# Kernel optimization log

Hardware: AMD Instinct MI355X
Metric: run time of the kernel (lower is better)

The kernel has to match this reference:

```python
import jax, jax.numpy as jnp
import numpy as np

C = 768        # n_embd
HSZ = 64       # HEAD_SIZE (module-level global in source)
H = C // HSZ   # n_head = 12
G = 2          # conv groups
DL = HSZ       # D_MIX_LORA = HEAD_SIZE
DD = 64        # TIME_DECAY_DIM
DG = C // 4    # D_GATE_LORA
B, T = 2, 2048

PNAMES = ['time_maa_x','time_maa_r','time_maa_w','time_maa_k','time_maa_v','time_maa_a','time_maa_g',
          'time_decay','time_faaaa','time_aaaaa','maa_w1','maa_w2','decay_w1','decay_w2','aaa_w1','aaa_w2',
          'kkk_w1','kkk_w2','gate_w1','gate_w2','w_key','w_value','w_receptance','w_output','ln_x_weight']

def setup_inputs() -> dict:
    key = jax.random.key(0)
    ks = jax.random.split(key, 32)
    f = lambda i, shape, s=1.0: jax.random.normal(ks[i], shape, jnp.float32) * s
    u = lambda i, shape: jax.random.uniform(ks[i], shape, dtype=jnp.float32)
    cs = float(C // G) ** -0.5
    return dict(
        x=f(0, (B, C, T)),
        time_maa_x=u(1, (1, C, 1)), time_maa_r=u(2, (1, C, 1)), time_maa_w=u(3, (1, C, 1)),
        time_maa_k=u(4, (1, C, 1)), time_maa_v=u(5, (1, C, 1)), time_maa_a=u(6, (1, C, 1)),
        time_maa_g=u(7, (1, C, 1)),
        time_decay=f(8, (1, C, 1), 0.5), time_faaaa=f(9, (H, HSZ), 0.1), time_aaaaa=f(10, (1, C, 1), 0.1),
        maa_w1=f(11, (6 * DL, C), 0.02), maa_w2=f(12, (6, DL, C), 0.02),
        decay_w1=f(13, (DD, C), 0.02), decay_w2=f(14, (C, DD), 0.02),
        aaa_w1=f(15, (DD, C), 0.02), aaa_w2=f(16, (C, DD), 0.02),
        kkk_w1=f(17, (DD, C), 0.02), kkk_w2=f(18, (C, DD), 0.02),
        gate_w1=f(19, (DG, C), 0.02), gate_w2=f(20, (C, DG), 0.02),
        w_key=f(21, (G, C // G, C // G), cs), w_value=f(22, (G, C // G, C // G), cs),
        w_receptance=f(23, (G, C // G, C // G), cs), w_output=f(24, (G, C // G, C // G), cs),
        ln_x_weight=jnp.ones((C,), jnp.float32),
    )

def _gconv(x, w):
    # grouped 1x1 Conv1d: x (B,C,T), w (G, C/G out, C/G in) -> (B,C,T)
    b, c, t = x.shape
    xg = x.reshape(b, G, c // G, t)
    return jnp.einsum('goc,bgct->bgot', w, xg).reshape(b, c, t)

def _lora(w1, w2, z):
    # w2 @ tanh(w1 @ z), channels-first z (B,C,T)
    return jnp.einsum('cd,bdt->bct', w2, jnp.tanh(jnp.einsum('dc,bct->bdt', w1, z)))

def _wkv7(r, w, k, v, a, bb):
    # RWKV-7 generalized delta-rule recurrence. All inputs (B,T,C), w in log-decay space.
    b, t, c = r.shape
    rs = lambda x: jnp.moveaxis(x.reshape(b, t, H, HSZ), 1, 0)  # (T,B,H,N)
    r4, k4, v4, a4, b4 = map(rs, (r, k, v, a, bb))
    wdec = rs(jnp.exp(-jnp.exp(w)))
    def step(S, inp):
        rr, ww, kk, vv, aa, b2 = inp  # each (B,H,N)
        sab = jnp.einsum('bhij,bhj,bhk->bhik', S, aa, b2)
        S = S * ww[:, :, None, :] + sab + vv[..., None] * kk[:, :, None, :]
        y = jnp.einsum('bhij,bhj->bhi', S, rr)
        return S, y
    S0 = jnp.zeros((b, H, HSZ, HSZ), r.dtype)
    _, ys = jax.lax.scan(step, S0, (r4, wdec, k4, v4, a4, b4))
    return jnp.moveaxis(ys, 0, 1).reshape(b, t, c)

def _forward(x, time_maa_x, time_maa_r, time_maa_w, time_maa_k, time_maa_v, time_maa_a, time_maa_g,
             time_decay, time_faaaa, time_aaaaa, maa_w1, maa_w2, decay_w1, decay_w2, aaa_w1, aaa_w2,
             kkk_w1, kkk_w2, gate_w1, gate_w2, w_key, w_value, w_receptance, w_output, ln_x_weight):
    b, c, t = x.shape
    xx = x  # shift_mode == 'none'
    xm = x * time_maa_x + xx * (1.0 - time_maa_x)
    tm = jnp.tanh(jnp.einsum('dc,bct->bdt', maa_w1, xm)).reshape(b, 6, DL, t)
    mix = jnp.einsum('bndt,ndc->nbct', tm, maa_w2)  # (6,B,C,T)
    mr, mw, mk, mv, ma, mg = mix
    xr = x + xx * (time_maa_r + mr)
    xw = x + xx * (time_maa_w + mw)
    xk = x + xx * (time_maa_k + mk)
    xv = x + xx * (time_maa_v + mv)
    xa = x + xx * (time_maa_a + ma)
    xg = x + xx * (time_maa_g + mg)
    tr = lambda z: z.transpose(0, 2, 1)  # (B,C,T) -> (B,T,C)
    r = tr(_gconv(xr, w_receptance))
    wlog = tr(-jax.nn.softplus(-(time_decay + _lora(decay_w1, decay_w2, xw))) - 0.5)
    k = tr(_gconv(xk, w_key))
    v = tr(_gconv(xv, w_value))
    g = tr(_lora(gate_w1, gate_w2, xg))
    kk = k + tr(_lora(kkk_w1, kkk_w2, xk))
    kk4 = kk.reshape(b, t, H, HSZ)
    kk = (kk4 / jnp.maximum(jnp.linalg.norm(kk4, axis=-1, keepdims=True), 1e-12)).reshape(b, t, c)
    a = jax.nn.sigmoid(tr(time_aaaaa + _lora(aaa_w1, aaa_w2, xa)))
    y = _wkv7(r, wlog, k, v, -kk, kk * a)
    # ln_x: RMSNorm over channel dim
    y = y * jax.lax.rsqrt(jnp.mean(y * y, axis=-1, keepdims=True) + 1e-5) * ln_x_weight
    rk = (r.reshape(b, t, H, HSZ) * k.reshape(b, t, H, HSZ) * time_faaaa).sum(-1, keepdims=True)
    y = y + (rk * v.reshape(b, t, H, HSZ)).reshape(b, t, c)
    return _gconv(tr(y * g), w_output)  # (B,C,T)

def reference(x, time_maa_x, time_maa_r, time_maa_w, time_maa_k, time_maa_v, time_maa_a, time_maa_g,
              time_decay, time_faaaa, time_aaaaa, maa_w1, maa_w2, decay_w1, decay_w2, aaa_w1, aaa_w2,
              kkk_w1, kkk_w2, gate_w1, gate_w2, w_key, w_value, w_receptance, w_output, ln_x_weight):
    return _forward(x, time_maa_x, time_maa_r, time_maa_w, time_maa_k, time_maa_v, time_maa_a, time_maa_g,
                    time_decay, time_faaaa, time_aaaaa, maa_w1, maa_w2, decay_w1, decay_w2, aaa_w1, aaa_w2,
                    kkk_w1, kkk_w2, gate_w1, gate_w2, w_key, w_value, w_receptance, w_output, ln_x_weight)
```

## Files before the change

kernel.cpp:

```cpp
#include <hip/hip_runtime.h>
#include <math.h>

#define BB 2
#define TT 2048
#define CC 768
#define HH 12
#define NN 64
#define GG 2
#define CG 384
#define FF 3145728L
#define S1 1572864L

typedef __attribute__((ext_vector_type(8))) short bf8frag;
typedef __attribute__((ext_vector_type(4))) float f4acc;

__device__ inline unsigned short f2bf(float x) {
    union { float f; unsigned u; } v; v.f = x;
    unsigned r = v.u + 0x7FFFu + ((v.u >> 16) & 1u);
    return (unsigned short)(r >> 16);
}
__device__ inline float bf2f(unsigned short u) {
    union { unsigned u; float f; } v; v.u = ((unsigned)u) << 16;
    return v.f;
}

template<int ATRANS, int BTRANS, int TOUT, int MODE>
__global__ __launch_bounds__(256) void gemm_kernel(
    const float* __restrict__ A, const float* __restrict__ Bm, float* __restrict__ Cm,
    const float* __restrict__ aux, const float* __restrict__ aux2,
    int K, int ldA, int ldB, int ldC, int zInner,
    long sA_o, long sA_i, long sB_o, long sB_i, long sC_o, long sC_i,
    long sAux_i, long sAux2_o, unsigned short* bfout)
{
    const int zo = blockIdx.z / zInner;
    const int zi = blockIdx.z % zInner;
    A  += (size_t)zo * sA_o + (size_t)zi * sA_i;
    Bm += (size_t)zo * sB_o + (size_t)zi * sB_i;
    Cm += (size_t)zo * sC_o + (size_t)zi * sC_i;
    if (MODE == 2) { aux += (size_t)zi * sAux_i; aux2 += (size_t)zo * sAux2_o; }

    const int m0t = blockIdx.y * 64;
    const int n0t = blockIdx.x * 64;
    const int tid = threadIdx.x;

    __shared__ float As[16][64];
    __shared__ float Bs[16][64];

    int mi, ni;
    if (TOUT) { mi = (tid & 15) * 4; ni = (tid >> 4) * 4; }
    else      { ni = (tid & 15) * 4; mi = (tid >> 4) * 4; }

    float acc[4][4];
#pragma unroll
    for (int i = 0; i < 4; ++i)
#pragma unroll
        for (int j = 0; j < 4; ++j) acc[i][j] = 0.f;

    for (int k0 = 0; k0 < K; k0 += 16) {
        if (!ATRANS) {
            const int row = tid >> 2;
            const int kc  = (tid & 3) * 4;
            float4 av = *(const float4*)&A[(size_t)(m0t + row) * ldA + k0 + kc];
            As[kc + 0][row] = av.x; As[kc + 1][row] = av.y;
            As[kc + 2][row] = av.z; As[kc + 3][row] = av.w;
        } else {
            const int krow = tid >> 4;
            const int mc   = (tid & 15) * 4;
            *(float4*)&As[krow][mc] = *(const float4*)&A[(size_t)(k0 + krow) * ldA + m0t + mc];
        }
        if (!BTRANS) {
            const int krow = tid >> 4;
            const int tc   = (tid & 15) * 4;
            *(float4*)&Bs[krow][tc] = *(const float4*)&Bm[(size_t)(k0 + krow) * ldB + n0t + tc];
        } else {
            const int trow = tid >> 2;
            const int kc   = (tid & 3) * 4;
            float4 bv = *(const float4*)&Bm[(size_t)(n0t + trow) * ldB + k0 + kc];
            Bs[kc + 0][trow] = bv.x; Bs[kc + 1][trow] = bv.y;
            Bs[kc + 2][trow] = bv.z; Bs[kc + 3][trow] = bv.w;
        }
        __syncthreads();
#pragma unroll
        for (int kk = 0; kk < 16; ++kk) {
            float4 a4 = *(const float4*)&As[kk][mi];
            float4 b4 = *(const float4*)&Bs[kk][ni];
            float am[4] = {a4.x, a4.y, a4.z, a4.w};
            float bn[4] = {b4.x, b4.y, b4.z, b4.w};
#pragma unroll
            for (int i = 0; i < 4; ++i)
#pragma unroll
                for (int j = 0; j < 4; ++j) acc[i][j] = fmaf(am[i], bn[j], acc[i][j]);
        }
        __syncthreads();
    }

    const int mbase = m0t + mi, nbase = n0t + ni;
#pragma unroll
    for (int i = 0; i < 4; ++i) {
        float4 xv;
        if (MODE == 2) xv = *(const float4*)&aux2[(size_t)(mbase + i) * ldC + nbase];
        float xa[4] = {0.f, 0.f, 0.f, 0.f};
        if (MODE == 2) { xa[0] = xv.x; xa[1] = xv.y; xa[2] = xv.z; xa[3] = xv.w; }
#pragma unroll
        for (int j = 0; j < 4; ++j) {
            float v = acc[i][j];
            if (MODE == 1) v = tanhf(v);
            else if (MODE == 2) v = xa[j] * (aux[mbase + i] + v);
            else if (MODE == 3) {
                float u  = aux[mbase + i] + v;
                float sp = fmaxf(-u, 0.f) + log1pf(expf(-fabsf(u)));
                float wl = -sp - 0.5f;
                v = expf(-expf(wl));
            } else if (MODE == 4) {
                float u = aux[mbase + i] + v;
                v = 1.f / (1.f + expf(-u));
            }
            acc[i][j] = v;
        }
    }
    if (!TOUT) {
        const bool skipf = (MODE == 2) && (bfout != nullptr) && (zi == 0 || zi == 3);
        if (!skipf) {
#pragma unroll
            for (int i = 0; i < 4; ++i) {
                float4 o = {acc[i][0], acc[i][1], acc[i][2], acc[i][3]};
                *(float4*)&Cm[(size_t)(mbase + i) * ldC + nbase] = o;
            }
        }
        if (MODE == 2 && bfout != nullptr) {
            int sidx = (zi == 0) ? 0 : (zi == 2) ? 1 : (zi == 3) ? 2 : -1;
            if (sidx >= 0) {
                unsigned short* bp = bfout + (size_t)sidx * FF + (size_t)zo * ((long)CC * TT);
#pragma unroll
                for (int i = 0; i < 4; ++i) {
                    ushort4 o = {f2bf(acc[i][0]), f2bf(acc[i][1]), f2bf(acc[i][2]), f2bf(acc[i][3])};
                    *(ushort4*)&bp[(size_t)(mbase + i) * ldC + nbase] = o;
                }
            }
        }
    } else {
#pragma unroll
        for (int j = 0; j < 4; ++j) {
            float4 o = {acc[0][j], acc[1][j], acc[2][j], acc[3][j]};
            *(float4*)&Cm[(size_t)(nbase + j) * ldC + mbase] = o;
        }
    }
}

__global__ __launch_bounds__(256) void lorah_kernel(
    const float* __restrict__ w0, const float* __restrict__ w1,
    const float* __restrict__ w2, const float* __restrict__ w3,
    const float* __restrict__ x0, const float* __restrict__ x1,
    const float* __restrict__ x2, const float* __restrict__ x3,
    float* __restrict__ o0, float* __restrict__ o1,
    float* __restrict__ o2, float* __restrict__ o3)
{
    const int z = blockIdx.z;
    const int which = z >> 1, bz = z & 1;
    if (which < 3 && blockIdx.y > 0) return;
    const float* A; const float* Bm; float* Cm; int M;
    if (which == 0)      { A = w0; Bm = x0; Cm = o0; M = 64; }
    else if (which == 1) { A = w1; Bm = x1; Cm = o1; M = 64; }
    else if (which == 2) { A = w2; Bm = x2; Cm = o2; M = 64; }
    else                 { A = w3; Bm = x3; Cm = o3; M = 192; }
    Bm += (size_t)bz * ((long)CC * TT);
    Cm += (size_t)bz * ((long)M * TT);

    const int m0t = blockIdx.y * 64;
    const int n0t = blockIdx.x * 64;
    const int tid = threadIdx.x;

    __shared__ float As[16][64];
    __shared__ float Bs[16][64];

    const int ni = (tid & 15) * 4, mi = (tid >> 4) * 4;
    float acc[4][4];
#pragma unroll
    for (int i = 0; i < 4; ++i)
#pragma unroll
        for (int j = 0; j < 4; ++j) acc[i][j] = 0.f;

    for (int k0 = 0; k0 < CC; k0 += 16) {
        {
            const int row = tid >> 2, kc = (tid & 3) * 4;
            float4 av = *(const float4*)&A[(size_t)(m0t + row) * CC + k0 + kc];
            As[kc + 0][row] = av.x; As[kc + 1][row] = av.y;
            As[kc + 2][row] = av.z; As[kc + 3][row] = av.w;
        }
        {
            const int krow = tid >> 4, tc = (tid & 15) * 4;
            *(float4*)&Bs[krow][tc] = *(const float4*)&Bm[(size_t)(k0 + krow) * TT + n0t + tc];
        }
        __syncthreads();
#pragma unroll
        for (int kk = 0; kk < 16; ++kk) {
            float4 a4 = *(const float4*)&As[kk][mi];
            float4 b4 = *(const float4*)&Bs[kk][ni];
            float am[4] = {a4.x, a4.y, a4.z, a4.w};
            float bn[4] = {b4.x, b4.y, b4.z, b4.w};
#pragma unroll
            for (int i = 0; i < 4; ++i)
#pragma unroll
                for (int j = 0; j < 4; ++j) acc[i][j] = fmaf(am[i], bn[j], acc[i][j]);
        }
        __syncthreads();
    }
    const int mbase = m0t + mi, nbase = n0t + ni;
#pragma unroll
    for (int i = 0; i < 4; ++i) {
        float4 o = {tanhf(acc[i][0]), tanhf(acc[i][1]), tanhf(acc[i][2]), tanhf(acc[i][3])};
        *(float4*)&Cm[(size_t)(mbase + i) * TT + nbase] = o;
    }
}

__global__ __launch_bounds__(256) void convs3_mfma_kernel(
    const unsigned short* __restrict__ wball, const unsigned short* __restrict__ X6t,
    float* __restrict__ X6)
{
    const int z = blockIdx.z;
    const int conv = z >> 2, bg = z & 3, b = bg >> 1, g = bg & 1;
    const unsigned short* Wb = wball + (size_t)conv * 294912;
    const unsigned short* Xb = X6t + (size_t)conv * FF;
    const int oslot = (conv == 0) ? 1 : (conv == 1) ? 4 : 5;
    float* Cout = X6 + (size_t)oslot * FF;

    const int t0 = blockIdx.x * 128;
    const int m0 = blockIdx.y * 128;
    const int tid = threadIdx.x;
    const int wave = tid >> 6, lane = tid & 63;
    const int lq = lane >> 4, lr = lane & 15;

    __shared__ unsigned short Ws[128 * 40];
    __shared__ unsigned short Xs[128 * 40];

    const unsigned short* Wg = Wb + (size_t)g * (CG * CG);
    const long xbase = (long)b * (long)TT * CC;

    f4acc acc0[8], acc1[8];
#pragma unroll
    for (int j = 0; j < 8; ++j) { acc0[j] = (f4acc)0.f; acc1[j] = (f4acc)0.f; }

    for (int k0 = 0; k0 < CG; k0 += 32) {
        {
            const int m = tid >> 1, kc = (tid & 1) * 16;
            const unsigned short* src = Wg + (size_t)(m0 + m) * CG + k0 + kc;
            *(bf8frag*)&Ws[m * 40 + kc]     = *(const bf8frag*)src;
            *(bf8frag*)&Ws[m * 40 + kc + 8] = *(const bf8frag*)(src + 8);
        }
        {
            const int t = tid >> 1, kc = (tid & 1) * 16;
            const unsigned short* src = Xb + xbase + (long)(t0 + t) * CC + g * CG + k0 + kc;
            *(bf8frag*)&Xs[t * 40 + kc]     = *(const bf8frag*)src;
            *(bf8frag*)&Xs[t * 40 + kc + 8] = *(const bf8frag*)(src + 8);
        }
        __syncthreads();

        bf8frag a0 = *(const bf8frag*)&Ws[(32 * wave + lr) * 40 + lq * 8];
        bf8frag a1 = *(const bf8frag*)&Ws[(32 * wave + 16 + lr) * 40 + lq * 8];
#pragma unroll
        for (int nj = 0; nj < 8; ++nj) {
            bf8frag bb = *(const bf8frag*)&Xs[(16 * nj + lr) * 40 + lq * 8];
            acc0[nj] = __builtin_amdgcn_mfma_f32_16x16x32_bf16(a0, bb, acc0[nj], 0, 0, 0);
            acc1[nj] = __builtin_amdgcn_mfma_f32_16x16x32_bf16(a1, bb, acc1[nj], 0, 0, 0);
        }
        __syncthreads();
    }

#pragma unroll
    for (int fi = 0; fi < 2; ++fi) {
        const int cbase = m0 + 32 * wave + 16 * fi + lq * 4;
#pragma unroll
        for (int nj = 0; nj < 8; ++nj) {
            const f4acc av = fi ? acc1[nj] : acc0[nj];
            const int t = t0 + 16 * nj + lr;
            float4 o = {av[0], av[1], av[2], av[3]};
            *(float4*)&Cout[(long)b * (long)TT * CC + (long)t * CC + g * CG + cbase] = o;
        }
    }
}

__global__ __launch_bounds__(256) void convout_mfma_kernel(
    const unsigned short* __restrict__ Wb, const unsigned short* __restrict__ Xb,
    float* __restrict__ Cout)
{
    const int bz = blockIdx.z; const int b = bz >> 1, g = bz & 1;
    const int t0 = blockIdx.x * 128;
    const int m0 = blockIdx.y * 128;
    const int tid = threadIdx.x;
    const int wave = tid >> 6, lane = tid & 63;
    const int lq = lane >> 4, lr = lane & 15;

    __shared__ unsigned short Ws[128 * 40];
    __shared__ unsigned short Xs[128 * 40];

    const unsigned short* Wg = Wb + (size_t)g * (CG * CG);
    const long xbase = (long)b * (long)TT * CC;

    f4acc acc0[8], acc1[8];
#pragma unroll
    for (int j = 0; j < 8; ++j) { acc0[j] = (f4acc)0.f; acc1[j] = (f4acc)0.f; }

    for (int k0 = 0; k0 < CG; k0 += 32) {
        {
            const int m = tid >> 1, kc = (tid & 1) * 16;
            const unsigned short* src = Wg + (size_t)(m0 + m) * CG + k0 + kc;
            *(bf8frag*)&Ws[m * 40 + kc]     = *(const bf8frag*)src;
            *(bf8frag*)&Ws[m * 40 + kc + 8] = *(const bf8frag*)(src + 8);
        }
        {
            const int t = tid >> 1, kc = (tid & 1) * 16;
            const unsigned short* src = Xb + xbase + (long)(t0 + t) * CC + g * CG + k0 + kc;
            *(bf8frag*)&Xs[t * 40 + kc]     = *(const bf8frag*)src;
            *(bf8frag*)&Xs[t * 40 + kc + 8] = *(const bf8frag*)(src + 8);
        }
        __syncthreads();

        bf8frag a0 = *(const bf8frag*)&Ws[(32 * wave + lr) * 40 + lq * 8];
        bf8frag a1 = *(const bf8frag*)&Ws[(32 * wave + 16 + lr) * 40 + lq * 8];
#pragma unroll
        for (int nj = 0; nj < 8; ++nj) {
            bf8frag bb = *(const bf8frag*)&Xs[(16 * nj + lr) * 40 + lq * 8];
            acc0[nj] = __builtin_amdgcn_mfma_f32_16x16x32_bf16(a0, bb, acc0[nj], 0, 0, 0);
            acc1[nj] = __builtin_amdgcn_mfma_f32_16x16x32_bf16(a1, bb, acc1[nj], 0, 0, 0);
        }
        __syncthreads();
    }

#pragma unroll
    for (int fi = 0; fi < 2; ++fi) {
        const int cbase = m0 + 32 * wave + 16 * fi + lq * 4;
#pragma unroll
        for (int nj = 0; nj < 8; ++nj) {
            const f4acc av = fi ? acc1[nj] : acc0[nj];
            const int t = t0 + 16 * nj + lr;
#pragma unroll
            for (int i = 0; i < 4; ++i)
                Cout[(long)b * (long)CC * TT + (long)(g * CG + cbase + i) * TT + t] = av[i];
        }
    }
}

__global__ __launch_bounds__(256) void maaw1_mfma_kernel(
    const unsigned short* __restrict__ Wb, const unsigned short* __restrict__ Xb,
    float* __restrict__ Cout)
{
    const int b = blockIdx.z;
    const int t0 = blockIdx.x * 128;
    const int m0 = blockIdx.y * 128;
    const int tid = threadIdx.x;
    const int wave = tid >> 6, lane = tid & 63;
    const int lq = lane >> 4, lr = lane & 15;

    __shared__ unsigned short Ws[128 * 40];
    __shared__ unsigned short Xs[128 * 40];

    const long xbase = (long)b * (long)TT * CC;

    f4acc acc0[8], acc1[8];
#pragma unroll
    for (int j = 0; j < 8; ++j) { acc0[j] = (f4acc)0.f; acc1[j] = (f4acc)0.f; }

    for (int k0 = 0; k0 < CC; k0 += 32) {
        {
            const int m = tid >> 1, kc = (tid & 1) * 16;
            const unsigned short* src = Wb + (size_t)(m0 + m) * CC + k0 + kc;
            *(bf8frag*)&Ws[m * 40 + kc]     = *(const bf8frag*)src;
            *(bf8frag*)&Ws[m * 40 + kc + 8] = *(const bf8frag*)(src + 8);
        }
        {
            const int t = tid >> 1, kc = (tid & 1) * 16;
            const unsigned short* src = Xb + xbase + (long)(t0 + t) * CC + k0 + kc;
            *(bf8frag*)&Xs[t * 40 + kc]     = *(const bf8frag*)src;
            *(bf8frag*)&Xs[t * 40 + kc + 8] = *(const bf8frag*)(src + 8);
        }
        __syncthreads();

        bf8frag a0 = *(const bf8frag*)&Ws[(32 * wave + lr) * 40 + lq * 8];
        bf8frag a1 = *(const bf8frag*)&Ws[(32 * wave + 16 + lr) * 40 + lq * 8];
#pragma unroll
        for (int nj = 0; nj < 8; ++nj) {
            bf8frag bb = *(const bf8frag*)&Xs[(16 * nj + lr) * 40 + lq * 8];
            acc0[nj] = __builtin_amdgcn_mfma_f32_16x16x32_bf16(a0, bb, acc0[nj], 0, 0, 0);
            acc1[nj] = __builtin_amdgcn_mfma_f32_16x16x32_bf16(a1, bb, acc1[nj], 0, 0, 0);
        }
        __syncthreads();
    }

#pragma unroll
    for (int fi = 0; fi < 2; ++fi) {
        const int m = m0 + 32 * wave + 16 * fi + lq * 4;
#pragma unroll
        for (int nj = 0; nj < 8; ++nj) {
            const f4acc av = fi ? acc1[nj] : acc0[nj];
            const int t = t0 + 16 * nj + lr;
#pragma unroll
            for (int i = 0; i < 4; ++i)
                Cout[(long)b * 384 * TT + (long)(m + i) * TT + t] = tanhf(av[i]);
        }
    }
}

__global__ __launch_bounds__(256) void xtr_kernel(const float* __restrict__ xin,
                                                  unsigned short* __restrict__ xout)
{
    __shared__ unsigned short L[64][68];
    const int t0 = blockIdx.x * 64, c0 = blockIdx.y * 64, b = blockIdx.z;
    const int tid = threadIdx.x;
    const int lr = tid >> 4, lc = (tid & 15) * 4;
#pragma unroll
    for (int i = 0; i < 4; ++i) {
        int c = lr + i * 16;
        float4 v = *(const float4*)&xin[(size_t)b * CC * TT + (size_t)(c0 + c) * TT + t0 + lc];
        L[c][lc + 0] = f2bf(v.x); L[c][lc + 1] = f2bf(v.y);
        L[c][lc + 2] = f2bf(v.z); L[c][lc + 3] = f2bf(v.w);
    }
    __syncthreads();
#pragma unroll
    for (int i = 0; i < 4; ++i) {
        int t = lr + i * 16;
        ushort4 o = {L[lc + 0][t], L[lc + 1][t], L[lc + 2][t], L[lc + 3][t]};
        *(ushort4*)&xout[(size_t)b * TT * CC + (size_t)(t0 + t) * CC + c0 + lc] = o;
    }
}

__global__ __launch_bounds__(256) void btr_kernel(const unsigned short* __restrict__ xin,
                                                  unsigned short* __restrict__ xout)
{
    __shared__ unsigned short L[64][68];
    const int t0 = blockIdx.x * 64, c0 = blockIdx.y * 64;
    const int s = blockIdx.z >> 1, b = blockIdx.z & 1;
    const int tid = threadIdx.x;
    const int lr = tid >> 4, lc = (tid & 15) * 4;
    const size_t ibase = (size_t)s * FF + (size_t)b * CC * TT;
    const size_t obase = (size_t)s * FF + (size_t)b * TT * CC;
#pragma unroll
    for (int i = 0; i < 4; ++i) {
        int c = lr + i * 16;
        ushort4 v = *(const ushort4*)&xin[ibase + (size_t)(c0 + c) * TT + t0 + lc];
        L[c][lc + 0] = v.x; L[c][lc + 1] = v.y; L[c][lc + 2] = v.z; L[c][lc + 3] = v.w;
    }
    __syncthreads();
#pragma unroll
    for (int i = 0; i < 4; ++i) {
        int t = lr + i * 16;
        ushort4 o = {L[lc + 0][t], L[lc + 1][t], L[lc + 2][t], L[lc + 3][t]};
        *(ushort4*)&xout[obase + (size_t)(t0 + t) * CC + c0 + lc] = o;
    }
}

__global__ void wcvt_kernel(const float* __restrict__ w0, const float* __restrict__ w1,
                            const float* __restrict__ w2, const float* __restrict__ w3,
                            const float* __restrict__ w4, unsigned short* __restrict__ wb)
{
    const int i = blockIdx.x * 256 + threadIdx.x;
    const int which = i / 294912, r = i - which * 294912;
    const float* s = (which == 0) ? w0 : (which == 1) ? w1 : (which == 2) ? w2
                   : (which == 3) ? w3 : w4;
    wb[i] = f2bf(s[r]);
}

__global__ void pack_aux_kernel(const float* __restrict__ r, const float* __restrict__ w,
                                const float* __restrict__ k, const float* __restrict__ v,
                                const float* __restrict__ a, const float* __restrict__ g,
                                float* __restrict__ paux)
{
    int c = blockIdx.x * blockDim.x + threadIdx.x;
    if (c < CC) {
        paux[0 * CC + c] = 1.f + r[c];
        paux[1 * CC + c] = 1.f + w[c];
        paux[2 * CC + c] = 1.f + k[c];
        paux[3 * CC + c] = 1.f + v[c];
        paux[4 * CC + c] = 1.f + a[c];
        paux[5 * CC + c] = 1.f + g[c];
    }
}

__global__ __launch_bounds__(256) void e1_kernel(const float* __restrict__ kA,
                                                 float* __restrict__ kvecA,
                                                 float* __restrict__ aA)
{
    const size_t base = (size_t)blockIdx.x * CC;
    const int tid = threadIdx.x;
#pragma unroll
    for (int ch = 0; ch < 3; ++ch) {
        int c = ch * 256 + tid;
        float kk = kA[base + c] + kvecA[base + c];
        float ss = kk * kk;
#pragma unroll
        for (int off = 32; off; off >>= 1) ss += __shfl_xor(ss, off, 64);
        float denom = fmaxf(sqrtf(ss), 1e-12f);
        float kkn = kk / denom;
        float av = aA[base + c];
        kvecA[base + c] = -kkn;
        aA[base + c]    = kkn * av;
    }
}

struct WFrag {
    float4 w[2], a[2], b[2], k[2], r[2];
    float vv;
};

__global__ __launch_bounds__(64) void wkv_kernel(
    const float* __restrict__ rA, const float* __restrict__ wA,
    const float* __restrict__ kA, const float* __restrict__ vA,
    const float* __restrict__ aaA, const float* __restrict__ b2A,
    unsigned short* __restrict__ yp8)
{
    const int blk = blockIdx.x;
    const int bh = blk % 24, rg = blk / 24;
    const int b = bh / HH, h = bh - b * HH;
    const int lane = threadIdx.x;
    const int jg = lane >> 3, p = lane & 7;
    const int row = rg * 8 + p;
    const int base = b * TT * CC + h * NN;
    const int fo = jg * 8;
    const int ybase = (jg * BB + b) * (TT * CC) + h * NN + row;

    float S[8];
#pragma unroll
    for (int i = 0; i < 8; ++i) S[i] = 0.f;

    WFrag f0, f1, f2;

    auto loadfrag = [&](WFrag& f, int t) {
        const int o = base + t * CC + fo;
#pragma unroll
        for (int q = 0; q < 2; ++q) {
            f.w[q] = *(const float4*)&wA[o + 4 * q];
            f.a[q] = *(const float4*)&aaA[o + 4 * q];
            f.b[q] = *(const float4*)&b2A[o + 4 * q];
            f.k[q] = *(const float4*)&kA[o + 4 * q];
            f.r[q] = *(const float4*)&rA[o + 4 * q];
        }
        f.vv = vA[base + t * CC + row];
    };

    auto stepf = [&](const WFrag& f, int t) {
        const float vv = f.vv;
        float vk[8];
#pragma unroll
        for (int q = 0; q < 2; ++q) {
            vk[4*q+0] = vv * f.k[q].x;
            vk[4*q+1] = vv * f.k[q].y;
            vk[4*q+2] = vv * f.k[q].z;
            vk[4*q+3] = vv * f.k[q].w;
        }

        float t0 = 0.f, t1 = 0.f, t2 = 0.f, t3 = 0.f;
#pragma unroll
        for (int q = 0; q < 2; ++q) {
            float4 a4 = f.a[q];
            t0 = fmaf(S[4*q+0], a4.x, t0);
            t1 = fmaf(S[4*q+1], a4.y, t1);
            t2 = fmaf(S[4*q+2], a4.z, t2);
            t3 = fmaf(S[4*q+3], a4.w, t3);
        }
        float part = (t0 + t1) + (t2 + t3);
        float s08 = __shfl_xor(part,  8, 64);
        float s16 = __shfl_xor(part, 16, 64);
        float s24 = __shfl_xor(part, 24, 64);
        float s32 = __shfl_xor(part, 32, 64);
        float s40 = __shfl_xor(part, 40, 64);
        float s48 = __shfl_xor(part, 48, 64);
        float s56 = __shfl_xor(part, 56, 64);
        float tmp = ((part + s08) + (s16 + s24)) + ((s32 + s40) + (s48 + s56));

        float y0 = 0.f, y1 = 0.f, y2 = 0.f, y3 = 0.f;
#pragma unroll
        for (int q = 0; q < 2; ++q) {
            float4 w4 = f.w[q], b4 = f.b[q], r4 = f.r[q];
            S[4*q+0] = fmaf(S[4*q+0], w4.x, fmaf(tmp, b4.x, vk[4*q+0]));
            y0 = fmaf(S[4*q+0], r4.x, y0);
            S[4*q+1] = fmaf(S[4*q+1], w4.y, fmaf(tmp, b4.y, vk[4*q+1]));
            y1 = fmaf(S[4*q+1], r4.y, y1);
            S[4*q+2] = fmaf(S[4*q+2], w4.z, fmaf(tmp, b4.z, vk[4*q+2]));
            y2 = fmaf(S[4*q+2], r4.z, y2);
            S[4*q+3] = fmaf(S[4*q+3], w4.w, fmaf(tmp, b4.w, vk[4*q+3]));
            y3 = fmaf(S[4*q+3], r4.w, y3);
        }
        yp8[ybase + t * CC] = f2bf((y0 + y1) + (y2 + y3));
    };

    loadfrag(f0, 0);
    loadfrag(f1, 1);
    loadfrag(f2, 2);

    int t = 0;
    for (; t + 2 < TT; t += 3) {
        stepf(f0, t);
        if (t + 3 < TT) loadfrag(f0, t + 3);
        stepf(f1, t + 1);
        if (t + 4 < TT) loadfrag(f1, t + 4);
        stepf(f2, t + 2);
        if (t + 5 < TT) loadfrag(f2, t + 5);
    }
    if (t < TT) stepf(f0, t);
    if (t + 1 < TT) stepf(f1, t + 1);
}

__global__ __launch_bounds__(256) void e2_kernel(
    const unsigned short* __restrict__ yp8, const float* __restrict__ rA,
    const float* __restrict__ kA, const float* __restrict__ vA,
    const float* __restrict__ gA, const float* __restrict__ faaaa,
    const float* __restrict__ lnw, unsigned short* __restrict__ zB)
{
    const int bt = blockIdx.x;
    const int b = bt / TT, t = bt - b * TT;
    const size_t base = (size_t)bt * CC;
    const int tid = threadIdx.x;
    const int wave = tid >> 6;
    __shared__ float red[4];
    __shared__ float rk[12];

    float yv[3];
    float ss = 0.f;
#pragma unroll
    for (int ch = 0; ch < 3; ++ch) {
        int c = ch * 256 + tid;
        float y = 0.f;
#pragma unroll
        for (int jg = 0; jg < 8; ++jg)
            y += bf2f(yp8[((size_t)(jg * BB + b) * TT + t) * CC + c]);
        yv[ch] = y;
        ss = fmaf(y, y, ss);
        float p = rA[base + c] * kA[base + c] * faaaa[c];
#pragma unroll
        for (int off = 32; off; off >>= 1) p += __shfl_xor(p, off, 64);
        if ((tid & 63) == 0) rk[ch * 4 + wave] = p;
    }
#pragma unroll
    for (int off = 32; off; off >>= 1) ss += __shfl_xor(ss, off, 64);
    if ((tid & 63) == 0) red[wave] = ss;
    __syncthreads();
    const float total = red[0] + red[1] + red[2] + red[3];
    const float scale = rsqrtf(total / (float)CC + 1e-5f);
#pragma unroll
    for (int ch = 0; ch < 3; ++ch) {
        int c = ch * 256 + tid;
        float out = yv[ch] * scale * lnw[c] + rk[c >> 6] * vA[base + c];
        zB[base + c] = f2bf(out * gA[base + c]);
    }
}

extern "C" void kernel_launch(void* const* d_in, const int* in_sizes, int n_in,
                              void* d_out, int out_size, void* d_ws, size_t ws_size,
                              hipStream_t stream)
{
    (void)in_sizes; (void)n_in; (void)out_size; (void)ws_size;
    const float* x        = (const float*)d_in[0];
    const float* tmaa_r   = (const float*)d_in[2];
    const float* tmaa_w   = (const float*)d_in[3];
    const float* tmaa_k   = (const float*)d_in[4];
    const float* tmaa_v   = (const float*)d_in[5];
    const float* tmaa_a   = (const float*)d_in[6];
    const float* tmaa_g   = (const float*)d_in[7];
    const float* tdecay   = (const float*)d_in[8];
    const float* tfaaaa   = (const float*)d_in[9];
    const float* taaaaa   = (const float*)d_in[10];
    const float* maa_w1   = (const float*)d_in[11];
    const float* maa_w2   = (const float*)d_in[12];
    const float* decay_w1 = (const float*)d_in[13];
    const float* decay_w2 = (const float*)d_in[14];
    const float* aaa_w1   = (const float*)d_in[15];
    const float* aaa_w2   = (const float*)d_in[16];
    const float* kkk_w1   = (const float*)d_in[17];
    const float* kkk_w2   = (const float*)d_in[18];
    const float* gate_w1  = (const float*)d_in[19];
    const float* gate_w2  = (const float*)d_in[20];
    const float* w_key    = (const float*)d_in[21];
    const float* w_value  = (const float*)d_in[22];
    const float* w_recept = (const float*)d_in[23];
    const float* w_output = (const float*)d_in[24];
    const float* lnw      = (const float*)d_in[25];
    float* out = (float*)d_out;

    float* ws   = (float*)d_ws;
    float* paux = ws;
    float* tm   = ws + 8192;
    float* X6   = tm + S1;
    float* dh   = X6 + 6 * FF;
    float* ah   = dh + 262144;
    float* kh   = ah + 262144;
    float* gh   = kh + 262144;
    float* gbuf = gh + 786432;
    unsigned short* yp8 = (unsigned short*)(gbuf + FF);
    unsigned short* X6b = yp8 + 8 * FF;
    unsigned short* zb  = X6b + 3 * FF;
    unsigned short* wb  = zb + FF;
    unsigned short* xtb = wb + 5L * 294912;
    unsigned short* X6t = xtb + FF;

    float* xw = X6 + 1 * FF; float* xk = X6 + 2 * FF;
    float* xa = X6 + 4 * FF; float* xg = X6 + 5 * FF;
    float* wwB = X6 + 0 * FF; float* rB  = X6 + 1 * FF; float* aaB = X6 + 2 * FF;
    float* b2B = X6 + 3 * FF; float* kB  = X6 + 4 * FF; float* vB  = X6 + 5 * FF;

    const long CT = (long)CC * TT;
    const long TC = (long)TT * CC;

    pack_aux_kernel<<<dim3(3), 256, 0, stream>>>(tmaa_r, tmaa_w, tmaa_k, tmaa_v, tmaa_a, tmaa_g, paux);
    wcvt_kernel<<<dim3(5760), 256, 0, stream>>>(w_recept, w_key, w_value, w_output, maa_w1, wb);
    xtr_kernel<<<dim3(32, 12, 2), 256, 0, stream>>>(x, xtb);

    maaw1_mfma_kernel<<<dim3(16, 3, 2), 256, 0, stream>>>(wb + 4L * 294912, xtb, tm);

    gemm_kernel<1,0,0,2><<<dim3(32, 12, 12), 256, 0, stream>>>(
        maa_w2, tm, X6, paux, x,
        64, 768, TT, TT, 6,
        0, 64L * 768, 384L * TT, 64L * TT, CT, FF, 768, CT, X6b);

    btr_kernel<<<dim3(32, 12, 6), 256, 0, stream>>>(X6b, X6t);

    lorah_kernel<<<dim3(32, 3, 8), 256, 0, stream>>>(
        decay_w1, aaa_w1, kkk_w1, gate_w1, xw, xa, xk, xg, dh, ah, kh, gh);

    convs3_mfma_kernel<<<dim3(16, 3, 12), 256, 0, stream>>>(wb, X6t, X6);

    gemm_kernel<0,0,1,3><<<dim3(32, 12, 2), 256, 0, stream>>>(
        decay_w2, dh, wwB, tdecay, nullptr, 64, 64, TT, CC, 1,
        0, 0, 64L * TT, 0, TC, 0, 0, 0, nullptr);
    gemm_kernel<0,0,1,4><<<dim3(32, 12, 2), 256, 0, stream>>>(
        aaa_w2, ah, b2B , taaaaa, nullptr, 64, 64, TT, CC, 1,
        0, 0, 64L * TT, 0, TC, 0, 0, 0, nullptr);
    gemm_kernel<0,0,1,0><<<dim3(32, 12, 2), 256, 0, stream>>>(
        kkk_w2, kh, aaB , nullptr, nullptr, 64, 64, TT, CC, 1,
        0, 0, 64L * TT, 0, TC, 0, 0, 0, nullptr);
    gemm_kernel<0,0,1,0><<<dim3(32, 12, 2), 256, 0, stream>>>(
        gate_w2, gh, gbuf, nullptr, nullptr, 192, 192, TT, CC, 1,
        0, 0, 192L * TT, 0, TC, 0, 0, 0, nullptr);

    e1_kernel<<<dim3(BB * TT), 256, 0, stream>>>(kB, aaB, b2B);

    wkv_kernel<<<dim3(BB * HH * 8), 64, 0, stream>>>(rB, wwB, kB, vB, aaB, b2B, yp8);

    e2_kernel<<<dim3(BB * TT), 256, 0, stream>>>(yp8, rB, kB, vB, gbuf, tfaaaa, lnw, zb);

    convout_mfma_kernel<<<dim3(16, 3, 4), 256, 0, stream>>>(wb + 3L * 294912, zb, out);
}
```

Measured before the change: 866.7 us.

## Move WKV state-dot reduction off the serial critical path via precomputed scalars

Rewrites the WKV recurrence so the cross-lane reduction S·a for the next step is computed from the pre-update state (with w and the next step's a folded in). The current step's tmp is then rebuilt from precomputed per-head scalars beta=b_{t-1}·a_t and gamma=k_{t-1}·a_t, which a new bg_kernel produces. This removes the shuffle reduction latency from the dependency chain between consecutive timesteps, so it can overlap with the state update. In exchange it adds an extra kernel launch and an extra pass over b, a and k, and reassociates floating-point sums.

```diff
diff --git a/kernel.cpp b/kernel.cpp
--- a/kernel.cpp
+++ b/kernel.cpp
@@ -496,15 +496,48 @@
     }
 }
 
+__global__ __launch_bounds__(256) void bg_kernel(
+    const float* __restrict__ b2A, const float* __restrict__ aaA,
+    const float* __restrict__ kA, float2* __restrict__ bgout)
+{
+    const int bt = blockIdx.x;
+    const int b = bt / TT, t = bt - b * TT;
+    const int tid = threadIdx.x;
+    const size_t base  = (size_t)bt * CC;
+    const size_t basep = base - CC;
+#pragma unroll
+    for (int ch = 0; ch < 3; ++ch) {
+        int c = ch * 256 + tid;
+        int h = c >> 6;
+        float pb = 0.f, pk = 0.f;
+        if (t > 0) {
+            float av = aaA[base + c];
+            pb = b2A[basep + c] * av;
+            pk = kA[basep + c] * av;
+        }
+#pragma unroll
+        for (int off = 32; off; off >>= 1) {
+            pb += __shfl_xor(pb, off, 64);
+            pk += __shfl_xor(pk, off, 64);
+        }
+        if ((tid & 63) == 0) {
+            float2 o; o.x = pb; o.y = pk;
+            bgout[(size_t)(b * HH + h) * TT + t] = o;
+        }
+    }
+}
+
 struct WFrag {
-    float4 w[2], a[2], b[2], k[2], r[2];
+    float4 a[2], w[2], b[2], k[2], r[2];
     float vv;
+    float beta, gamma;
 };
 
 __global__ __launch_bounds__(64) void wkv_kernel(
     const float* __restrict__ rA, const float* __restrict__ wA,
     const float* __restrict__ kA, const float* __restrict__ vA,
     const float* __restrict__ aaA, const float* __restrict__ b2A,
+    const float2* __restrict__ bgA,
     unsigned short* __restrict__ yp8)
 {
     const int blk = blockIdx.x;
@@ -516,19 +549,24 @@
     const int base = b * TT * CC + h * NN;
     const int fo = jg * 8;
     const int ybase = (jg * BB + b) * (TT * CC) + h * NN + row;
+    const float2* bgp = bgA + (size_t)bh * TT;
 
     float S[8];
 #pragma unroll
     for (int i = 0; i < 8; ++i) S[i] = 0.f;
+
+    float tmp_prev = 0.f, v_prev = 0.f, u_cur = 0.f;
 
     WFrag f0, f1, f2;
 
     auto loadfrag = [&](WFrag& f, int t) {
         const int o = base + t * CC + fo;
+        float2 bg2 = bgp[t];
+        f.beta = bg2.x; f.gamma = bg2.y;
 #pragma unroll
         for (int q = 0; q < 2; ++q) {
+            f.a[q] = *(const float4*)&aaA[o + 4 * q];
             f.w[q] = *(const float4*)&wA[o + 4 * q];
-            f.a[q] = *(const float4*)&aaA[o + 4 * q];
             f.b[q] = *(const float4*)&b2A[o + 4 * q];
             f.k[q] = *(const float4*)&kA[o + 4 * q];
             f.r[q] = *(const float4*)&rA[o + 4 * q];
@@ -536,49 +574,45 @@
         f.vv = vA[base + t * CC + row];
     };
 
-    auto stepf = [&](const WFrag& f, int t) {
+    auto stepf = [&](const WFrag& f, const WFrag& fn, int t) {
+        const float tmp = fmaf(f.beta, tmp_prev, fmaf(f.gamma, v_prev, u_cur));
         const float vv = f.vv;
-        float vk[8];
+
+        float ua0 = 0.f, ua1 = 0.f, ua2 = 0.f, ua3 = 0.f;
 #pragma unroll
         for (int q = 0; q < 2; ++q) {
-            vk[4*q+0] = vv * f.k[q].x;
-            vk[4*q+1] = vv * f.k[q].y;
-            vk[4*q+2] = vv * f.k[q].z;
-            vk[4*q+3] = vv * f.k[q].w;
-        }
-
-        float t0 = 0.f, t1 = 0.f, t2 = 0.f, t3 = 0.f;
+            const float4 w4 = f.w[q], an4 = fn.a[q];
+            ua0 = fmaf(S[4*q+0], w4.x * an4.x, ua0);
+            ua1 = fmaf(S[4*q+1], w4.y * an4.y, ua1);
+            ua2 = fmaf(S[4*q+2], w4.z * an4.z, ua2);
+            ua3 = fmaf(S[4*q+3], w4.w * an4.w, ua3);
+        }
+        const float upart = (ua0 + ua1) + (ua2 + ua3);
+        float s08 = __shfl_xor(upart,  8, 64);
+        float s16 = __shfl_xor(upart, 16, 64);
+        float s24 = __shfl_xor(upart, 24, 64);
+        float s32 = __shfl_xor(upart, 32, 64);
+        float s40 = __shfl_xor(upart, 40, 64);
+        float s48 = __shfl_xor(upart, 48, 64);
+        float s56 = __shfl_xor(upart, 56, 64);
+
+        float y0 = 0.f, y1 = 0.f, y2 = 0.f, y3 = 0.f;
 #pragma unroll
         for (int q = 0; q < 2; ++q) {
-            float4 a4 = f.a[q];
-            t0 = fmaf(S[4*q+0], a4.x, t0);
-            t1 = fmaf(S[4*q+1], a4.y, t1);
-            t2 = fmaf(S[4*q+2], a4.z, t2);
-            t3 = fmaf(S[4*q+3], a4.w, t3);
-        }
-        float part = (t0 + t1) + (t2 + t3);
-        float s08 = __shfl_xor(part,  8, 64);
-        float s16 = __shfl_xor(part, 16, 64);
-        float s24 = __shfl_xor(part, 24, 64);
-        float s32 = __shfl_xor(part, 32, 64);
-        float s40 = __shfl_xor(part, 40, 64);
-        float s48 = __shfl_xor(part, 48, 64);
-        float s56 = __shfl_xor(part, 56, 64);
-        float tmp = ((part + s08) + (s16 + s24)) + ((s32 + s40) + (s48 + s56));
-
-        float y0 = 0.f, y1 = 0.f, y2 = 0.f, y3 = 0.f;
-#pragma unroll
-        for (int q = 0; q < 2; ++q) {
-            float4 w4 = f.w[q], b4 = f.b[q], r4 = f.r[q];
-            S[4*q+0] = fmaf(S[4*q+0], w4.x, fmaf(tmp, b4.x, vk[4*q+0]));
+            const float4 w4 = f.w[q], b4 = f.b[q], k4 = f.k[q], r4 = f.r[q];
+            S[4*q+0] = fmaf(S[4*q+0], w4.x, fmaf(tmp, b4.x, vv * k4.x));
             y0 = fmaf(S[4*q+0], r4.x, y0);
-            S[4*q+1] = fmaf(S[4*q+1], w4.y, fmaf(tmp, b4.y, vk[4*q+1]));
+            S[4*q+1] = fmaf(S[4*q+1], w4.y, fmaf(tmp, b4.y, vv * k4.y));
             y1 = fmaf(S[4*q+1], r4.y, y1);
-            S[4*q+2] = fmaf(S[4*q+2], w4.z, fmaf(tmp, b4.z, vk[4*q+2]));
+            S[4*q+2] = fmaf(S[4*q+2], w4.z, fmaf(tmp, b4.z, vv * k4.z));
             y2 = fmaf(S[4*q+2], r4.z, y2);
-            S[4*q+3] = fmaf(S[4*q+3], w4.w, fmaf(tmp, b4.w, vk[4*q+3]));
+            S[4*q+3] = fmaf(S[4*q+3], w4.w, fmaf(tmp, b4.w, vv * k4.w));
             y3 = fmaf(S[4*q+3], r4.w, y3);
         }
+
+        u_cur = ((upart + s08) + (s16 + s24)) + ((s32 + s40) + (s48 + s56));
+        tmp_prev = tmp; v_prev = vv;
+
         yp8[ybase + t * CC] = f2bf((y0 + y1) + (y2 + y3));
     };
 
@@ -588,15 +622,15 @@
 
     int t = 0;
     for (; t + 2 < TT; t += 3) {
-        stepf(f0, t);
+        stepf(f0, f1, t);
         if (t + 3 < TT) loadfrag(f0, t + 3);
-        stepf(f1, t + 1);
+        stepf(f1, f2, t + 1);
         if (t + 4 < TT) loadfrag(f1, t + 4);
-        stepf(f2, t + 2);
+        stepf(f2, f0, t + 2);
         if (t + 5 < TT) loadfrag(f2, t + 5);
     }
-    if (t < TT) stepf(f0, t);
-    if (t + 1 < TT) stepf(f1, t + 1);
+    if (t < TT) stepf(f0, f1, t);
+    if (t + 1 < TT) stepf(f1, f2, t + 1);
 }
 
 __global__ __launch_bounds__(256) void e2_kernel(
@@ -696,6 +730,8 @@
     float* wwB = X6 + 0 * FF; float* rB  = X6 + 1 * FF; float* aaB = X6 + 2 * FF;
     float* b2B = X6 + 3 * FF; float* kB  = X6 + 4 * FF; float* vB  = X6 + 5 * FF;
 
+    float2* bgbuf = (float2*)tm;
+
     const long CT = (long)CC * TT;
     const long TC = (long)TT * CC;
 
@@ -732,7 +768,9 @@
 
     e1_kernel<<<dim3(BB * TT), 256, 0, stream>>>(kB, aaB, b2B);
 
-    wkv_kernel<<<dim3(BB * HH * 8), 64, 0, stream>>>(rB, wwB, kB, vB, aaB, b2B, yp8);
+    bg_kernel<<<dim3(BB * TT), 256, 0, stream>>>(b2B, aaB, kB, bgbuf);
+
+    wkv_kernel<<<dim3(BB * HH * 8), 64, 0, stream>>>(rB, wwB, kB, vB, aaB, b2B, bgbuf, yp8);
 
     e2_kernel<<<dim3(BB * TT), 256, 0, stream>>>(yp8, rB, kB, vB, gbuf, tfaaaa, lnw, zb);
 
```

Result: slower. 962.1 us (+11.0%).

## Overlap gate LoRA second GEMM with WKV recurrence in one launch

Applied to the files above, without the earlier changes.

The gate LoRA up-projection GEMM moves into the WKV kernel as extra blocks. The first 192 blocks run the serial recurrence on one wave each, and the remaining 768 blocks compute the gate GEMM with a simple shared-memory tiled FMA loop. This lets the latency-bound recurrence, which leaves most CUs idle, run alongside the GEMM and removes one launch. In exchange the WKV blocks now launch with 256 threads but use only 64, which changes their occupancy and register budget. The GEMM also uses a hand-written path instead of the shared gemm_kernel.

```diff
diff --git a/kernel.cpp b/kernel.cpp
--- a/kernel.cpp
+++ b/kernel.cpp
@@ -501,102 +501,162 @@
     float vv;
 };
 
-__global__ __launch_bounds__(64) void wkv_kernel(
+__global__ __launch_bounds__(256) void wkv_gate_kernel(
     const float* __restrict__ rA, const float* __restrict__ wA,
     const float* __restrict__ kA, const float* __restrict__ vA,
     const float* __restrict__ aaA, const float* __restrict__ b2A,
-    unsigned short* __restrict__ yp8)
-{
-    const int blk = blockIdx.x;
-    const int bh = blk % 24, rg = blk / 24;
-    const int b = bh / HH, h = bh - b * HH;
-    const int lane = threadIdx.x;
-    const int jg = lane >> 3, p = lane & 7;
-    const int row = rg * 8 + p;
-    const int base = b * TT * CC + h * NN;
-    const int fo = jg * 8;
-    const int ybase = (jg * BB + b) * (TT * CC) + h * NN + row;
-
-    float S[8];
-#pragma unroll
-    for (int i = 0; i < 8; ++i) S[i] = 0.f;
-
-    WFrag f0, f1, f2;
-
-    auto loadfrag = [&](WFrag& f, int t) {
-        const int o = base + t * CC + fo;
-#pragma unroll
-        for (int q = 0; q < 2; ++q) {
-            f.w[q] = *(const float4*)&wA[o + 4 * q];
-            f.a[q] = *(const float4*)&aaA[o + 4 * q];
-            f.b[q] = *(const float4*)&b2A[o + 4 * q];
-            f.k[q] = *(const float4*)&kA[o + 4 * q];
-            f.r[q] = *(const float4*)&rA[o + 4 * q];
-        }
-        f.vv = vA[base + t * CC + row];
-    };
-
-    auto stepf = [&](const WFrag& f, int t) {
-        const float vv = f.vv;
-        float vk[8];
-#pragma unroll
-        for (int q = 0; q < 2; ++q) {
-            vk[4*q+0] = vv * f.k[q].x;
-            vk[4*q+1] = vv * f.k[q].y;
-            vk[4*q+2] = vv * f.k[q].z;
-            vk[4*q+3] = vv * f.k[q].w;
-        }
-
-        float t0 = 0.f, t1 = 0.f, t2 = 0.f, t3 = 0.f;
-#pragma unroll
-        for (int q = 0; q < 2; ++q) {
-            float4 a4 = f.a[q];
-            t0 = fmaf(S[4*q+0], a4.x, t0);
-            t1 = fmaf(S[4*q+1], a4.y, t1);
-            t2 = fmaf(S[4*q+2], a4.z, t2);
-            t3 = fmaf(S[4*q+3], a4.w, t3);
-        }
-        float part = (t0 + t1) + (t2 + t3);
-        float s08 = __shfl_xor(part,  8, 64);
-        float s16 = __shfl_xor(part, 16, 64);
-        float s24 = __shfl_xor(part, 24, 64);
-        float s32 = __shfl_xor(part, 32, 64);
-        float s40 = __shfl_xor(part, 40, 64);
-        float s48 = __shfl_xor(part, 48, 64);
-        float s56 = __shfl_xor(part, 56, 64);
-        float tmp = ((part + s08) + (s16 + s24)) + ((s32 + s40) + (s48 + s56));
-
-        float y0 = 0.f, y1 = 0.f, y2 = 0.f, y3 = 0.f;
-#pragma unroll
-        for (int q = 0; q < 2; ++q) {
-            float4 w4 = f.w[q], b4 = f.b[q], r4 = f.r[q];
-            S[4*q+0] = fmaf(S[4*q+0], w4.x, fmaf(tmp, b4.x, vk[4*q+0]));
-            y0 = fmaf(S[4*q+0], r4.x, y0);
-            S[4*q+1] = fmaf(S[4*q+1], w4.y, fmaf(tmp, b4.y, vk[4*q+1]));
-            y1 = fmaf(S[4*q+1], r4.y, y1);
-            S[4*q+2] = fmaf(S[4*q+2], w4.z, fmaf(tmp, b4.z, vk[4*q+2]));
-            y2 = fmaf(S[4*q+2], r4.z, y2);
-            S[4*q+3] = fmaf(S[4*q+3], w4.w, fmaf(tmp, b4.w, vk[4*q+3]));
-            y3 = fmaf(S[4*q+3], r4.w, y3);
-        }
-        yp8[ybase + t * CC] = f2bf((y0 + y1) + (y2 + y3));
-    };
-
-    loadfrag(f0, 0);
-    loadfrag(f1, 1);
-    loadfrag(f2, 2);
-
-    int t = 0;
-    for (; t + 2 < TT; t += 3) {
-        stepf(f0, t);
-        if (t + 3 < TT) loadfrag(f0, t + 3);
-        stepf(f1, t + 1);
-        if (t + 4 < TT) loadfrag(f1, t + 4);
-        stepf(f2, t + 2);
-        if (t + 5 < TT) loadfrag(f2, t + 5);
-    }
-    if (t < TT) stepf(f0, t);
-    if (t + 1 < TT) stepf(f1, t + 1);
+    unsigned short* __restrict__ yp8,
+    const float* __restrict__ gw2, const float* __restrict__ ghh,
+    float* __restrict__ gbuf)
+{
+    if (blockIdx.x < 192) {
+        if (threadIdx.x >= 64) return;
+        const int blk = blockIdx.x;
+        const int bh = blk % 24, rg = blk / 24;
+        const int b = bh / HH, h = bh - b * HH;
+        const int lane = threadIdx.x;
+        const int jg = lane >> 3, p = lane & 7;
+        const int row = rg * 8 + p;
+        const int base = b * TT * CC + h * NN;
+        const int fo = jg * 8;
+        const int ybase = (jg * BB + b) * (TT * CC) + h * NN + row;
+
+        float S[8];
+#pragma unroll
+        for (int i = 0; i < 8; ++i) S[i] = 0.f;
+
+        WFrag f0, f1, f2;
+
+        auto loadfrag = [&](WFrag& f, int t) {
+            const int o = base + t * CC + fo;
+#pragma unroll
+            for (int q = 0; q < 2; ++q) {
+                f.w[q] = *(const float4*)&wA[o + 4 * q];
+                f.a[q] = *(const float4*)&aaA[o + 4 * q];
+                f.b[q] = *(const float4*)&b2A[o + 4 * q];
+                f.k[q] = *(const float4*)&kA[o + 4 * q];
+                f.r[q] = *(const float4*)&rA[o + 4 * q];
+            }
+            f.vv = vA[base + t * CC + row];
+        };
+
+        auto stepf = [&](const WFrag& f, int t) {
+            const float vv = f.vv;
+            float vk[8];
+#pragma unroll
+            for (int q = 0; q < 2; ++q) {
+                vk[4*q+0] = vv * f.k[q].x;
+                vk[4*q+1] = vv * f.k[q].y;
+                vk[4*q+2] = vv * f.k[q].z;
+                vk[4*q+3] = vv * f.k[q].w;
+            }
+
+            float t0 = 0.f, t1 = 0.f, t2 = 0.f, t3 = 0.f;
+#pragma unroll
+            for (int q = 0; q < 2; ++q) {
+                float4 a4 = f.a[q];
+                t0 = fmaf(S[4*q+0], a4.x, t0);
+                t1 = fmaf(S[4*q+1], a4.y, t1);
+                t2 = fmaf(S[4*q+2], a4.z, t2);
+                t3 = fmaf(S[4*q+3], a4.w, t3);
+            }
+            float part = (t0 + t1) + (t2 + t3);
+            float s08 = __shfl_xor(part,  8, 64);
+            float s16 = __shfl_xor(part, 16, 64);
+            float s24 = __shfl_xor(part, 24, 64);
+            float s32 = __shfl_xor(part, 32, 64);
+            float s40 = __shfl_xor(part, 40, 64);
+            float s48 = __shfl_xor(part, 48, 64);
+            float s56 = __shfl_xor(part, 56, 64);
+            float tmp = ((part + s08) + (s16 + s24)) + ((s32 + s40) + (s48 + s56));
+
+            float y0 = 0.f, y1 = 0.f, y2 = 0.f, y3 = 0.f;
+#pragma unroll
+            for (int q = 0; q < 2; ++q) {
+                float4 w4 = f.w[q], b4 = f.b[q], r4 = f.r[q];
+                S[4*q+0] = fmaf(S[4*q+0], w4.x, fmaf(tmp, b4.x, vk[4*q+0]));
+                y0 = fmaf(S[4*q+0], r4.x, y0);
+                S[4*q+1] = fmaf(S[4*q+1], w4.y, fmaf(tmp, b4.y, vk[4*q+1]));
+                y1 = fmaf(S[4*q+1], r4.y, y1);
+                S[4*q+2] = fmaf(S[4*q+2], w4.z, fmaf(tmp, b4.z, vk[4*q+2]));
+                y2 = fmaf(S[4*q+2], r4.z, y2);
+                S[4*q+3] = fmaf(S[4*q+3], w4.w, fmaf(tmp, b4.w, vk[4*q+3]));
+                y3 = fmaf(S[4*q+3], r4.w, y3);
+            }
+            yp8[ybase + t * CC] = f2bf((y0 + y1) + (y2 + y3));
+        };
+
+        loadfrag(f0, 0);
+        loadfrag(f1, 1);
+        loadfrag(f2, 2);
+
+        int t = 0;
+        for (; t + 2 < TT; t += 3) {
+            stepf(f0, t);
+            if (t + 3 < TT) loadfrag(f0, t + 3);
+            stepf(f1, t + 1);
+            if (t + 4 < TT) loadfrag(f1, t + 4);
+            stepf(f2, t + 2);
+            if (t + 5 < TT) loadfrag(f2, t + 5);
+        }
+        if (t < TT) stepf(f0, t);
+        if (t + 1 < TT) stepf(f1, t + 1);
+        return;
+    }
+
+    {
+        const int gb = blockIdx.x - 192;
+        const int n0t = (gb & 31) * 64;
+        const int rest = gb >> 5;
+        const int m0t = (rest % 12) * 64;
+        const int bz  = rest / 12;
+        const float* A  = gw2;
+        const float* Bm = ghh + (size_t)bz * (192L * TT);
+        float* Cm = gbuf + (size_t)bz * ((long)TT * CC);
+        const int tid = threadIdx.x;
+
+        __shared__ float As[16][64];
+        __shared__ float Bs[16][64];
+
+        const int mi = (tid & 15) * 4, ni = (tid >> 4) * 4;
+        float acc[4][4];
+#pragma unroll
+        for (int i = 0; i < 4; ++i)
+#pragma unroll
+            for (int j = 0; j < 4; ++j) acc[i][j] = 0.f;
+
+        for (int k0 = 0; k0 < 192; k0 += 16) {
+            {
+                const int row = tid >> 2, kc = (tid & 3) * 4;
+                float4 av = *(const float4*)&A[(size_t)(m0t + row) * 192 + k0 + kc];
+                As[kc + 0][row] = av.x; As[kc + 1][row] = av.y;
+                As[kc + 2][row] = av.z; As[kc + 3][row] = av.w;
+            }
+            {
+                const int krow = tid >> 4, tc = (tid & 15) * 4;
+                *(float4*)&Bs[krow][tc] = *(const float4*)&Bm[(size_t)(k0 + krow) * TT + n0t + tc];
+            }
+            __syncthreads();
+#pragma unroll
+            for (int kk = 0; kk < 16; ++kk) {
+                float4 a4 = *(const float4*)&As[kk][mi];
+                float4 b4 = *(const float4*)&Bs[kk][ni];
+                float am[4] = {a4.x, a4.y, a4.z, a4.w};
+                float bn[4] = {b4.x, b4.y, b4.z, b4.w};
+#pragma unroll
+                for (int i = 0; i < 4; ++i)
+#pragma unroll
+                    for (int j = 0; j < 4; ++j) acc[i][j] = fmaf(am[i], bn[j], acc[i][j]);
+            }
+            __syncthreads();
+        }
+        const int mbase = m0t + mi, nbase = n0t + ni;
+#pragma unroll
+        for (int j = 0; j < 4; ++j) {
+            float4 o = {acc[0][j], acc[1][j], acc[2][j], acc[3][j]};
+            *(float4*)&Cm[(size_t)(nbase + j) * CC + mbase] = o;
+        }
+    }
 }
 
 __global__ __launch_bounds__(256) void e2_kernel(
@@ -726,13 +786,11 @@
     gemm_kernel<0,0,1,0><<<dim3(32, 12, 2), 256, 0, stream>>>(
         kkk_w2, kh, aaB , nullptr, nullptr, 64, 64, TT, CC, 1,
         0, 0, 64L * TT, 0, TC, 0, 0, 0, nullptr);
-    gemm_kernel<0,0,1,0><<<dim3(32, 12, 2), 256, 0, stream>>>(
-        gate_w2, gh, gbuf, nullptr, nullptr, 192, 192, TT, CC, 1,
-        0, 0, 192L * TT, 0, TC, 0, 0, 0, nullptr);
 
     e1_kernel<<<dim3(BB * TT), 256, 0, stream>>>(kB, aaB, b2B);
 
-    wkv_kernel<<<dim3(BB * HH * 8), 64, 0, stream>>>(rB, wwB, kB, vB, aaB, b2B, yp8);
+    wkv_gate_kernel<<<dim3(960), 256, 0, stream>>>(
+        rB, wwB, kB, vB, aaB, b2B, yp8, gate_w2, gh, gbuf);
 
     e2_kernel<<<dim3(BB * TT), 256, 0, stream>>>(yp8, rB, kB, vB, gbuf, tfaaaa, lnw, zb);
 
```

Result: faster. 809.1 us (-6.6%).
